# Performance work log

Hardware: AMD Instinct MI355X
Metric: run time of the kernel (lower is better)

The kernel has to match this reference:

```python
import math
import jax, jax.numpy as jnp
import numpy as np

H, DK = 16, 64            # n_heads, d_kv
NUM_BUCKETS, MAX_DIST = 32, 128


def _relative_position_buckets(S):
    # Bidirectional (encoder) T5 bucketization of relative positions.
    ctx = jnp.arange(S, dtype=jnp.int32)[:, None]      # query positions
    mem = jnp.arange(S, dtype=jnp.int32)[None, :]      # key positions
    rp = mem - ctx                                     # [S, S]
    nb = NUM_BUCKETS // 2
    rb = (rp > 0).astype(jnp.int32) * nb
    n = jnp.abs(rp)
    max_exact = nb // 2
    is_small = n < max_exact
    large = max_exact + (
        jnp.log(jnp.maximum(n, 1).astype(jnp.float32) / max_exact)
        / math.log(MAX_DIST / max_exact)
        * (nb - max_exact)
    ).astype(jnp.int32)
    large = jnp.minimum(large, nb - 1)
    return rb + jnp.where(is_small, n, large)          # [S, S] int32


def setup_inputs() -> dict:
    key = jax.random.key(0)
    ks = jax.random.split(key, 6)
    B, S, D = 4, 1024, 1024
    inner = H * DK
    std = 0.02
    return {
        "hidden_states": jax.random.normal(ks[0], (B, S, D), jnp.float32),
        "Wq": jax.random.normal(ks[1], (inner, D), jnp.float32) * std,
        "Wk": jax.random.normal(ks[2], (inner, D), jnp.float32) * std,
        "Wv": jax.random.normal(ks[3], (inner, D), jnp.float32) * std,
        "Wo": jax.random.normal(ks[4], (D, inner), jnp.float32) * std,
        "rel_bias": jax.random.normal(ks[5], (NUM_BUCKETS, H), jnp.float32) * std,
    }


def reference(hidden_states, Wq, Wk, Wv, Wo, rel_bias):
    B, S, D = hidden_states.shape

    def proj(W):  # bias-free linear + split heads -> [B, H, S, DK]
        return (hidden_states @ W.T).reshape(B, S, H, DK).transpose(0, 2, 1, 3)

    q, k, v = proj(Wq), proj(Wk), proj(Wv)
    # T5: NO 1/sqrt(d) scaling
    scores = jnp.einsum("bhqd,bhkd->bhqk", q, k)       # [B, H, S, S]
    bias = rel_bias[_relative_position_buckets(S)]     # [S, S, H]
    scores = scores + bias.transpose(2, 0, 1)[None]    # broadcast over batch
    attn = jax.nn.softmax(scores, axis=-1)
    ctx = jnp.einsum("bhqk,bhkd->bhqd", attn, v)       # [B, H, S, DK]
    ctx = ctx.transpose(0, 2, 1, 3).reshape(B, S, H * DK)
    return ctx @ Wo.T                                  # [B, S, D]
```

## Files before the change

### kernel.cpp

```cpp
#include <hip/hip_runtime.h>

typedef _Float16 half8 __attribute__((ext_vector_type(8)));
typedef _Float16 half4_t __attribute__((ext_vector_type(4)));
typedef float f32x4 __attribute__((ext_vector_type(4)));

#define GK 1024
#define MEG (1024 * 1024)

#define GLD16(gptr, lptr) \
    __builtin_amdgcn_global_load_lds((const __attribute__((address_space(1))) void*)(gptr), \
                                     (__attribute__((address_space(3))) void*)(lptr), 16, 0, 0)

__global__ void cvt_all_kernel(const float* __restrict__ hidden,
                               const float* __restrict__ Wq,
                               const float* __restrict__ Wk,
                               const float* __restrict__ Wv,
                               const float* __restrict__ Wo,
                               _Float16* __restrict__ ws) {
    int b = blockIdx.x;
    const float* src;
    _Float16* dst;
    if (b < 4096)      { src = hidden; dst = ws; }
    else if (b < 5120) { src = Wq; dst = ws + 4 * MEG; b -= 4096; }
    else if (b < 6144) { src = Wk; dst = ws + 5 * MEG; b -= 5120; }
    else if (b < 7168) { src = Wv; dst = ws + 6 * MEG; b -= 6144; }
    else               { src = Wo; dst = ws + 7 * MEG; b -= 7168; }
    int i = (b * 256 + threadIdx.x) * 4;
    f32x4 v = *(const f32x4*)(src + i);
    half4_t h;
    h[0] = (_Float16)v[0]; h[1] = (_Float16)v[1];
    h[2] = (_Float16)v[2]; h[3] = (_Float16)v[3];
    *(half4_t*)(dst + i) = h;
}

template<int MODE>
__global__ __launch_bounds__(256) void gemm_kernel(
    const _Float16* __restrict__ A,
    const _Float16* __restrict__ B0,
    const _Float16* __restrict__ B1,
    const _Float16* __restrict__ B2,
    _Float16* __restrict__ O0,
    _Float16* __restrict__ O1,
    _Float16* __restrict__ O2,
    float* __restrict__ Of)
{
    const _Float16* Bw = B0;
    _Float16* Oh = O0;
    if (MODE == 0) {
        int z = blockIdx.z;
        Bw = (z == 0) ? B0 : ((z == 1) ? B1 : B2);
        Oh = (z == 0) ? O0 : ((z == 1) ? O1 : O2);
    }
    __shared__ __attribute__((aligned(16))) _Float16 sA[2][128][32];
    __shared__ __attribute__((aligned(16))) _Float16 sB[2][128][32];

    const int tid = threadIdx.x;
    const int wave = tid >> 6, lane = tid & 63;
    const int quad = lane >> 4, l16 = lane & 15;
    const int wr = wave >> 1, wc = wave & 1;
    const int M0 = blockIdx.y * 128, N0 = blockIdx.x * 128;

    const int rl = lane >> 2;
    const int cl = (lane & 3) * 8;
    const size_t aRow0 = (size_t)(M0 + wave * 16 + rl) * GK + cl;
    const size_t aRow1 = aRow0 + (size_t)64 * GK;
    const size_t bRow0 = (size_t)(N0 + wave * 16 + rl) * GK + cl;
    const size_t bRow1 = bRow0 + (size_t)64 * GK;
    _Float16* ldsA[2][2] = {{&sA[0][wave * 16][0], &sA[0][64 + wave * 16][0]},
                            {&sA[1][wave * 16][0], &sA[1][64 + wave * 16][0]}};
    _Float16* ldsB[2][2] = {{&sB[0][wave * 16][0], &sB[0][64 + wave * 16][0]},
                            {&sB[1][wave * 16][0], &sB[1][64 + wave * 16][0]}};

    f32x4 acc[4][4] = {};

    for (int kt = 0; kt < GK / 64; ++kt) {
        const int ko = kt * 64;
        #pragma unroll
        for (int c = 0; c < 2; ++c) {
            GLD16(A + aRow0 + ko + c * 32, ldsA[c][0]);
            GLD16(A + aRow1 + ko + c * 32, ldsA[c][1]);
            GLD16(Bw + bRow0 + ko + c * 32, ldsB[c][0]);
            GLD16(Bw + bRow1 + ko + c * 32, ldsB[c][1]);
        }
        __syncthreads();
        #pragma unroll
        for (int c = 0; c < 2; ++c) {
            half8 af[4], bf[4];
            #pragma unroll
            for (int i = 0; i < 4; ++i)
                af[i] = *(const half8*)&sA[c][wr * 64 + i * 16 + l16][quad * 8];
            #pragma unroll
            for (int j = 0; j < 4; ++j)
                bf[j] = *(const half8*)&sB[c][wc * 64 + j * 16 + l16][quad * 8];
            #pragma unroll
            for (int i = 0; i < 4; ++i)
                #pragma unroll
                for (int j = 0; j < 4; ++j)
                    acc[i][j] = __builtin_amdgcn_mfma_f32_16x16x32_f16(af[i], bf[j], acc[i][j], 0, 0, 0);
        }
        __syncthreads();
    }

    #pragma unroll
    for (int i = 0; i < 4; ++i) {
        #pragma unroll
        for (int j = 0; j < 4; ++j) {
            #pragma unroll
            for (int r = 0; r < 4; ++r) {
                int m = M0 + wr * 64 + i * 16 + quad * 4 + r;
                int n = N0 + wc * 64 + j * 16 + l16;
                float v = acc[i][j][r];
                if (MODE == 0) {
                    int b = m >> 10, s = m & 1023, hh = n >> 6, d = n & 63;
                    Oh[((size_t)((b * 16 + hh) * 1024 + s)) * 64 + d] = (_Float16)v;
                } else {
                    Of[(size_t)m * 1024 + n] = v;
                }
            }
        }
    }
}

__global__ __launch_bounds__(256) void transpose_v_kernel(
    const _Float16* __restrict__ V, _Float16* __restrict__ VT) {
    __shared__ _Float16 tile[64][65];
    const int s0 = blockIdx.x * 64;
    const int bh = blockIdx.y;
    const _Float16* Vb = V + (size_t)bh * 1024 * 64;
    _Float16* Tb = VT + (size_t)bh * 64 * 1024;
    const int tr = threadIdx.x >> 6;
    const int tc = threadIdx.x & 63;
    #pragma unroll
    for (int i = 0; i < 16; ++i) {
        int r = i * 4 + tr;
        tile[r][tc] = Vb[(size_t)(s0 + r) * 64 + tc];
    }
    __syncthreads();
    #pragma unroll
    for (int i = 0; i < 16; ++i) {
        int d = i * 4 + tr;
        Tb[(size_t)d * 1024 + s0 + tc] = tile[tc][d];
    }
}

__global__ __launch_bounds__(256) void attn_kernel(
    const _Float16* __restrict__ Q,
    const _Float16* __restrict__ K,
    const _Float16* __restrict__ VT,
    const float* __restrict__ rel_bias,
    _Float16* __restrict__ ctx)
{
    const int S = 1024;
    const int qt = blockIdx.x;
    const int q0 = qt * 64;
    const int h = blockIdx.y;
    const int b = blockIdx.z;
    const int bh = b * 16 + h;
    const _Float16* Qh = Q + (size_t)bh * S * 64;
    const _Float16* Kh = K + (size_t)bh * S * 64;
    const _Float16* VTh = VT + (size_t)bh * 64 * S;

    __shared__ __attribute__((aligned(16))) _Float16 sQ[64][72];
    __shared__ __attribute__((aligned(16))) _Float16 sK[64][72];
    __shared__ __attribute__((aligned(16))) _Float16 sVt[64][72];
    __shared__ __attribute__((aligned(16))) _Float16 sP[4][16][72];
    __shared__ _Float16 sBias[1088];

    const int tid = threadIdx.x;
    const int wave = tid >> 6, lane = tid & 63;
    const int quad = lane >> 4, l16 = lane & 15;

    {
        int r = tid >> 3, c = (tid & 7) * 8;
        *(half8*)&sQ[r][c]      = *(const half8*)(Qh + (size_t)(q0 + r) * 64 + c);
        *(half8*)&sQ[r + 32][c] = *(const half8*)(Qh + (size_t)(q0 + r + 32) * 64 + c);
    }
    for (int i = tid; i < 1087; i += 256) {
        int delta = i - (q0 + 63);
        int rb = (delta > 0) ? 16 : 0;
        int n = (delta < 0) ? -delta : delta;
        int bucket;
        if (n < 8) bucket = rb + n;
        else bucket = rb + 8 + (n >= 12) + (n >= 16) + (n >= 23) + (n >= 32)
                             + (n >= 46) + (n >= 64) + (n >= 91);
        sBias[i] = (_Float16)rel_bias[bucket * 16 + h];
    }
    __syncthreads();

    half8 qf0 = *(const half8*)&sQ[wave * 16 + l16][quad * 8];
    half8 qf1 = *(const half8*)&sQ[wave * 16 + l16][32 + quad * 8];

    float m_run = -INFINITY, l_run = 0.0f;
    f32x4 acc[4] = {};

    for (int kt = 0; kt < 16; ++kt) {
        __syncthreads();
        {
            int r = tid >> 3, c = (tid & 7) * 8;
            *(half8*)&sK[r][c]      = *(const half8*)(Kh + (size_t)(kt * 64 + r) * 64 + c);
            *(half8*)&sK[r + 32][c] = *(const half8*)(Kh + (size_t)(kt * 64 + r + 32) * 64 + c);
            *(half8*)&sVt[r][c]      = *(const half8*)(VTh + (size_t)r * S + kt * 64 + c);
            *(half8*)&sVt[r + 32][c] = *(const half8*)(VTh + (size_t)(r + 32) * S + kt * 64 + c);
        }
        __syncthreads();

        f32x4 sc[4] = {};
        #pragma unroll
        for (int j = 0; j < 4; ++j) {
            half8 kf0 = *(const half8*)&sK[j * 16 + l16][quad * 8];
            half8 kf1 = *(const half8*)&sK[j * 16 + l16][32 + quad * 8];
            sc[j] = __builtin_amdgcn_mfma_f32_16x16x32_f16(kf0, qf0, sc[j], 0, 0, 0);
            sc[j] = __builtin_amdgcn_mfma_f32_16x16x32_f16(kf1, qf1, sc[j], 0, 0, 0);
        }

        const int bbase = kt * 64 + quad * 4 - wave * 16 - l16 + 63;
        if (kt <= qt - 3 || kt >= qt + 3) {
            const float cb = (float)sBias[bbase];
            #pragma unroll
            for (int j = 0; j < 4; ++j)
                #pragma unroll
                for (int r = 0; r < 4; ++r)
                    sc[j][r] += cb;
        } else {
            #pragma unroll
            for (int j = 0; j < 4; ++j)
                #pragma unroll
                for (int r = 0; r < 4; ++r)
                    sc[j][r] += (float)sBias[bbase + j * 16 + r];
        }

        float mx = fmaxf(fmaxf(fmaxf(sc[0][0], sc[0][1]), fmaxf(sc[0][2], sc[0][3])),
                         fmaxf(fmaxf(sc[1][0], sc[1][1]), fmaxf(sc[1][2], sc[1][3])));
        mx = fmaxf(mx, fmaxf(fmaxf(fmaxf(sc[2][0], sc[2][1]), fmaxf(sc[2][2], sc[2][3])),
                             fmaxf(fmaxf(sc[3][0], sc[3][1]), fmaxf(sc[3][2], sc[3][3]))));
        mx = fmaxf(mx, __shfl_xor(mx, 16));
        mx = fmaxf(mx, __shfl_xor(mx, 32));
        float mnew = fmaxf(m_run, mx);
        float alpha = __expf(m_run - mnew);
        m_run = mnew;

        float ps = 0.0f;
        #pragma unroll
        for (int j = 0; j < 4; ++j) {
            half4_t pw;
            #pragma unroll
            for (int r = 0; r < 4; ++r) {
                float p = __expf(sc[j][r] - mnew);
                ps += p;
                pw[r] = (_Float16)p;
            }
            *(half4_t*)&sP[wave][l16][j * 16 + quad * 4] = pw;
        }
        l_run = l_run * alpha + ps;
        #pragma unroll
        for (int dt = 0; dt < 4; ++dt) acc[dt] *= alpha;
        __syncthreads();

        half8 pf0 = *(const half8*)&sP[wave][l16][quad * 8];
        half8 pf1 = *(const half8*)&sP[wave][l16][32 + quad * 8];
        #pragma unroll
        for (int dt = 0; dt < 4; ++dt) {
            half8 vf0 = *(const half8*)&sVt[dt * 16 + l16][quad * 8];
            half8 vf1 = *(const half8*)&sVt[dt * 16 + l16][32 + quad * 8];
            acc[dt] = __builtin_amdgcn_mfma_f32_16x16x32_f16(vf0, pf0, acc[dt], 0, 0, 0);
            acc[dt] = __builtin_amdgcn_mfma_f32_16x16x32_f16(vf1, pf1, acc[dt], 0, 0, 0);
        }
    }

    l_run += __shfl_xor(l_run, 16);
    l_run += __shfl_xor(l_run, 32);
    const float inv = 1.0f / l_run;
    const size_t qg = (size_t)(b * 1024 + q0 + wave * 16 + l16);
    #pragma unroll
    for (int dt = 0; dt < 4; ++dt) {
        half4_t o;
        #pragma unroll
        for (int r = 0; r < 4; ++r) o[r] = (_Float16)(acc[dt][r] * inv);
        *(half4_t*)&ctx[qg * 1024 + h * 64 + dt * 16 + quad * 4] = o;
    }
}

extern "C" void kernel_launch(void* const* d_in, const int* in_sizes, int n_in,
                              void* d_out, int out_size, void* d_ws, size_t ws_size,
                              hipStream_t stream) {
    const float* hidden   = (const float*)d_in[0];
    const float* Wq       = (const float*)d_in[1];
    const float* Wk       = (const float*)d_in[2];
    const float* Wv       = (const float*)d_in[3];
    const float* Wo       = (const float*)d_in[4];
    const float* rel_bias = (const float*)d_in[5];
    float* out = (float*)d_out;

    _Float16* ws    = (_Float16*)d_ws;
    _Float16* h16   = ws;
    _Float16* wq16  = ws + 4 * (size_t)MEG;
    _Float16* wk16  = ws + 5 * (size_t)MEG;
    _Float16* wv16  = ws + 6 * (size_t)MEG;
    _Float16* wo16  = ws + 7 * (size_t)MEG;
    _Float16* Qs    = ws + 8 * (size_t)MEG;
    _Float16* Ks    = ws + 12 * (size_t)MEG;
    _Float16* Vs    = ws + 16 * (size_t)MEG;
    _Float16* ctx16 = ws + 20 * (size_t)MEG;
    _Float16* VTs   = h16;

    cvt_all_kernel<<<8192, 256, 0, stream>>>(hidden, Wq, Wk, Wv, Wo, ws);

    gemm_kernel<0><<<dim3(8, 32, 3), 256, 0, stream>>>(
        h16, wq16, wk16, wv16, Qs, Ks, Vs, nullptr);

    transpose_v_kernel<<<dim3(16, 64), 256, 0, stream>>>(Vs, VTs);

    attn_kernel<<<dim3(16, 16, 4), 256, 0, stream>>>(Qs, Ks, VTs, rel_bias, ctx16);

    gemm_kernel<1><<<dim3(8, 32, 1), 256, 0, stream>>>(
        ctx16, wo16, nullptr, nullptr, nullptr, nullptr, nullptr, out);
}
```

Baseline: 206.7 us.

## Split output GEMM into smaller-tile kernel and trim attention loop sync

Replaces the templated GEMM with a dedicated QKV kernel and a separate output-projection kernel that uses 64x128 tiles. This doubles the block count for the 256-block output GEMM so more CUs are occupied. In the attention kernel, K/V load pointers are hoisted out of the loop and the barrier between writing and reading the per-wave P buffer is removed, relying on each wave touching only its own slice. Dropping that barrier risks a missing intra-wave ordering guarantee, but it cuts one sync per tile.

```diff
diff --git a/kernel.cpp b/kernel.cpp
--- a/kernel.cpp
+++ b/kernel.cpp
@@ -33,24 +33,19 @@
     *(half4_t*)(dst + i) = h;
 }
 
-template<int MODE>
-__global__ __launch_bounds__(256) void gemm_kernel(
+__global__ __launch_bounds__(256) void gemm_qkv_kernel(
     const _Float16* __restrict__ A,
     const _Float16* __restrict__ B0,
     const _Float16* __restrict__ B1,
     const _Float16* __restrict__ B2,
     _Float16* __restrict__ O0,
     _Float16* __restrict__ O1,
-    _Float16* __restrict__ O2,
-    float* __restrict__ Of)
+    _Float16* __restrict__ O2)
 {
-    const _Float16* Bw = B0;
-    _Float16* Oh = O0;
-    if (MODE == 0) {
-        int z = blockIdx.z;
-        Bw = (z == 0) ? B0 : ((z == 1) ? B1 : B2);
-        Oh = (z == 0) ? O0 : ((z == 1) ? O1 : O2);
-    }
+    int z = blockIdx.z;
+    const _Float16* Bw = (z == 0) ? B0 : ((z == 1) ? B1 : B2);
+    _Float16* Oh = (z == 0) ? O0 : ((z == 1) ? O1 : O2);
+
     __shared__ __attribute__((aligned(16))) _Float16 sA[2][128][32];
     __shared__ __attribute__((aligned(16))) _Float16 sB[2][128][32];
 
@@ -109,13 +104,73 @@
             for (int r = 0; r < 4; ++r) {
                 int m = M0 + wr * 64 + i * 16 + quad * 4 + r;
                 int n = N0 + wc * 64 + j * 16 + l16;
-                float v = acc[i][j][r];
-                if (MODE == 0) {
-                    int b = m >> 10, s = m & 1023, hh = n >> 6, d = n & 63;
-                    Oh[((size_t)((b * 16 + hh) * 1024 + s)) * 64 + d] = (_Float16)v;
-                } else {
-                    Of[(size_t)m * 1024 + n] = v;
-                }
+                int b = m >> 10, s = m & 1023, hh = n >> 6, d = n & 63;
+                Oh[((size_t)((b * 16 + hh) * 1024 + s)) * 64 + d] = (_Float16)acc[i][j][r];
+            }
+        }
+    }
+}
+
+__global__ __launch_bounds__(256) void gemm_o_kernel(
+    const _Float16* __restrict__ A,
+    const _Float16* __restrict__ Bw,
+    float* __restrict__ Of)
+{
+    __shared__ __attribute__((aligned(16))) _Float16 sA[2][64][32];
+    __shared__ __attribute__((aligned(16))) _Float16 sB[2][128][32];
+
+    const int tid = threadIdx.x;
+    const int wave = tid >> 6, lane = tid & 63;
+    const int quad = lane >> 4, l16 = lane & 15;
+    const int M0 = blockIdx.y * 64, N0 = blockIdx.x * 128;
+
+    const int rl = lane >> 2;
+    const int cl = (lane & 3) * 8;
+    const size_t aRow  = (size_t)(M0 + wave * 16 + rl) * GK + cl;
+    const size_t bRow0 = (size_t)(N0 + wave * 16 + rl) * GK + cl;
+    const size_t bRow1 = bRow0 + (size_t)64 * GK;
+    _Float16* ldsA[2]    = {&sA[0][wave * 16][0], &sA[1][wave * 16][0]};
+    _Float16* ldsB[2][2] = {{&sB[0][wave * 16][0], &sB[0][64 + wave * 16][0]},
+                            {&sB[1][wave * 16][0], &sB[1][64 + wave * 16][0]}};
+
+    f32x4 acc[4][2] = {};
+
+    for (int kt = 0; kt < GK / 64; ++kt) {
+        const int ko = kt * 64;
+        #pragma unroll
+        for (int c = 0; c < 2; ++c) {
+            GLD16(A + aRow + ko + c * 32, ldsA[c]);
+            GLD16(Bw + bRow0 + ko + c * 32, ldsB[c][0]);
+            GLD16(Bw + bRow1 + ko + c * 32, ldsB[c][1]);
+        }
+        __syncthreads();
+        #pragma unroll
+        for (int c = 0; c < 2; ++c) {
+            half8 af[4], bf[2];
+            #pragma unroll
+            for (int i = 0; i < 4; ++i)
+                af[i] = *(const half8*)&sA[c][i * 16 + l16][quad * 8];
+            #pragma unroll
+            for (int j = 0; j < 2; ++j)
+                bf[j] = *(const half8*)&sB[c][wave * 32 + j * 16 + l16][quad * 8];
+            #pragma unroll
+            for (int i = 0; i < 4; ++i)
+                #pragma unroll
+                for (int j = 0; j < 2; ++j)
+                    acc[i][j] = __builtin_amdgcn_mfma_f32_16x16x32_f16(af[i], bf[j], acc[i][j], 0, 0, 0);
+        }
+        __syncthreads();
+    }
+
+    #pragma unroll
+    for (int i = 0; i < 4; ++i) {
+        #pragma unroll
+        for (int j = 0; j < 2; ++j) {
+            #pragma unroll
+            for (int r = 0; r < 4; ++r) {
+                int m = M0 + i * 16 + quad * 4 + r;
+                int n = N0 + wave * 32 + j * 16 + l16;
+                Of[(size_t)m * 1024 + n] = acc[i][j][r];
             }
         }
     }
@@ -190,18 +245,27 @@
     half8 qf0 = *(const half8*)&sQ[wave * 16 + l16][quad * 8];
     half8 qf1 = *(const half8*)&sQ[wave * 16 + l16][32 + quad * 8];
 
+    const int sr = tid >> 3;
+    const int sc_ = (tid & 7) * 8;
+    const _Float16* kp0 = Kh + (size_t)sr * 64 + sc_;
+    const _Float16* kp1 = kp0 + (size_t)32 * 64;
+    const _Float16* vp0 = VTh + (size_t)sr * S + sc_;
+    const _Float16* vp1 = vp0 + (size_t)32 * S;
+    _Float16* sKw0 = &sK[sr][sc_];
+    _Float16* sKw1 = &sK[sr + 32][sc_];
+    _Float16* sVw0 = &sVt[sr][sc_];
+    _Float16* sVw1 = &sVt[sr + 32][sc_];
+
     float m_run = -INFINITY, l_run = 0.0f;
     f32x4 acc[4] = {};
 
     for (int kt = 0; kt < 16; ++kt) {
         __syncthreads();
-        {
-            int r = tid >> 3, c = (tid & 7) * 8;
-            *(half8*)&sK[r][c]      = *(const half8*)(Kh + (size_t)(kt * 64 + r) * 64 + c);
-            *(half8*)&sK[r + 32][c] = *(const half8*)(Kh + (size_t)(kt * 64 + r + 32) * 64 + c);
-            *(half8*)&sVt[r][c]      = *(const half8*)(VTh + (size_t)r * S + kt * 64 + c);
-            *(half8*)&sVt[r + 32][c] = *(const half8*)(VTh + (size_t)(r + 32) * S + kt * 64 + c);
-        }
+        *(half8*)sKw0 = *(const half8*)kp0;
+        *(half8*)sKw1 = *(const half8*)kp1;
+        *(half8*)sVw0 = *(const half8*)vp0;
+        *(half8*)sVw1 = *(const half8*)vp1;
+        kp0 += 4096; kp1 += 4096; vp0 += 64; vp1 += 64;
         __syncthreads();
 
         f32x4 sc[4] = {};
@@ -254,7 +318,6 @@
         l_run = l_run * alpha + ps;
         #pragma unroll
         for (int dt = 0; dt < 4; ++dt) acc[dt] *= alpha;
-        __syncthreads();
 
         half8 pf0 = *(const half8*)&sP[wave][l16][quad * 8];
         half8 pf1 = *(const half8*)&sP[wave][l16][32 + quad * 8];
@@ -305,13 +368,12 @@
 
     cvt_all_kernel<<<8192, 256, 0, stream>>>(hidden, Wq, Wk, Wv, Wo, ws);
 
-    gemm_kernel<0><<<dim3(8, 32, 3), 256, 0, stream>>>(
-        h16, wq16, wk16, wv16, Qs, Ks, Vs, nullptr);
+    gemm_qkv_kernel<<<dim3(8, 32, 3), 256, 0, stream>>>(
+        h16, wq16, wk16, wv16, Qs, Ks, Vs);
 
     transpose_v_kernel<<<dim3(16, 64), 256, 0, stream>>>(Vs, VTs);
 
     attn_kernel<<<dim3(16, 16, 4), 256, 0, stream>>>(Qs, Ks, VTs, rel_bias, ctx16);
 
-    gemm_kernel<1><<<dim3(8, 32, 1), 256, 0, stream>>>(
-        ctx16, wo16, nullptr, nullptr, nullptr, nullptr, nullptr, out);
-}
+    gemm_o_kernel<<<dim3(8, 64), 256, 0, stream>>>(ctx16, wo16, out);
+}
```

Result: faster. 200.4 us (-3.1%).
